# Performance work log

Hardware: AMD Instinct MI355X
Metric: run time of the kernel (lower is better)

## Reference

```python
import jax, jax.numpy as jnp
import numpy as np

E = 262144      # number of edges (triples)
D = 256         # embed_dim
DOUT = 256      # embed_out_dim
NQ = 65536      # num_query (output nodes)
NK = 65536      # num_key
ALPHA = 0.2     # leaky relu slope
EPS = 1e-12


def setup_inputs() -> dict:
    key = jax.random.key(0)
    ks = jax.random.split(key, 7)
    return {
        "key_list": jax.random.randint(ks[0], (E,), 0, NK),
        "key_embed": jax.random.normal(ks[1], (E, D), jnp.float32),
        "query_list": jax.random.randint(ks[2], (E,), 0, NQ),
        "query_embed": jax.random.normal(ks[3], (E, D), jnp.float32),
        # learned parameters (xavier-ish scale)
        "a": jax.random.normal(ks[4], (DOUT, 2 * D), jnp.float32) * 0.05,
        "a_2": jax.random.normal(ks[5], (1, DOUT), jnp.float32) * 0.05,
        "trans": jax.random.normal(ks[6], (DOUT, D), jnp.float32) * 0.05,
    }


def reference(key_list, key_embed, query_list, query_embed, a, a_2, trans):
    # edge_associated_set = trans @ key_embed.T, kept as (E, DOUT)
    edge_assoc = key_embed @ trans.T                              # (E, DOUT)
    # edge_m = a @ cat(key, query).T, kept as (E, DOUT)
    edge_h = jnp.concatenate([key_embed, query_embed], axis=1)    # (E, 2D)
    edge_m = edge_h @ a.T                                         # (E, DOUT)
    powers = -jax.nn.leaky_relu(edge_m @ a_2[0], negative_slope=ALPHA)  # (E,)
    edge_e = jnp.exp(powers)                                      # (E,) unnormalized attn
    # sparse COO sum over key dim == segment-sum by query index
    e_rowsum = jax.ops.segment_sum(edge_e, query_list, num_segments=NQ)[:, None]  # (NQ,1)
    e_rowsum = jnp.where(e_rowsum == 0.0, EPS, e_rowsum)
    # dropout p=0.0 (eval) -> identity
    edge_w = edge_e[:, None] * edge_assoc                         # (E, DOUT)
    h_prime = jax.ops.segment_sum(edge_w, query_list, num_segments=NQ)  # (NQ, DOUT)
    h_prime = h_prime / e_rowsum
    return jax.nn.elu(h_prime)  # concat=True branch
```

## Files before the change

### kernel.cpp

```cpp
#include <hip/hip_runtime.h>
#include <hip/hip_bf16.h>
#include <math.h>

namespace {
constexpr int kD = 256;
constexpr int kDOUT = 256;
constexpr int kNQ = 65536;
constexpr int kE = 262144;
constexpr float kAlpha = 0.2f;
constexpr float kEps = 1e-12f;
constexpr int kCap = 16;
constexpr int kOvfMax = 4096;
}

typedef short bf16x8 __attribute__((ext_vector_type(8)));
typedef float f32x4 __attribute__((ext_vector_type(4)));
typedef unsigned short u16x8 __attribute__((ext_vector_type(8)));

__global__ void compute_c_kernel(const float* __restrict__ a,
                                 const float* __restrict__ a2,
                                 float* __restrict__ c) {
  const int j = blockIdx.x * blockDim.x + threadIdx.x;
  float s = 0.f;
#pragma unroll 8
  for (int k = 0; k < kDOUT; ++k) s = fmaf(a[k * (2 * kD) + j], a2[k], s);
  c[j] = s;
}

__global__ void zero_kernel(int4* __restrict__ p, int* __restrict__ ovf_n) {
  p[blockIdx.x * 256 + threadIdx.x] = int4{0, 0, 0, 0};
  if (blockIdx.x == 0 && threadIdx.x == 0) *ovf_n = 0;
}

__global__ void cvt_trans_kernel(const float* __restrict__ t, ushort* __restrict__ tb) {
  const int i = blockIdx.x * 256 + threadIdx.x;
  const float4 v = reinterpret_cast<const float4*>(t)[i];
  union { ushort4 u; __hip_bfloat16 h[4]; } p;
  p.h[0] = __float2bfloat16(v.x);
  p.h[1] = __float2bfloat16(v.y);
  p.h[2] = __float2bfloat16(v.z);
  p.h[3] = __float2bfloat16(v.w);
  reinterpret_cast<ushort4*>(tb)[i] = p.u;
}

__global__ __launch_bounds__(256) void qdot_bin_kernel(
    const float* __restrict__ query_embed,
    const int* __restrict__ qlist,
    const float* __restrict__ c,
    int* __restrict__ count,
    int2* __restrict__ bins,
    int* __restrict__ ovf_n,
    int* __restrict__ ovf_q,
    int* __restrict__ ovf_e,
    float* __restrict__ ovf_qd) {
  const int wid = threadIdx.x >> 6;
  const int lane = threadIdx.x & 63;
  const int g = lane >> 4;
  const int l4 = lane & 15;
  const int edge = blockIdx.x * 16 + wid * 4 + g;

  int q = 0;
  if (l4 == 0) q = qlist[edge];

  const float4* qr = reinterpret_cast<const float4*>(query_embed) + (size_t)edge * 64 + l4 * 4;
  const float4 r0 = qr[0], r1 = qr[1], r2 = qr[2], r3 = qr[3];
  const float4 c0 = reinterpret_cast<const float4*>(c)[64 + l4 * 4 + 0];
  const float4 c1 = reinterpret_cast<const float4*>(c)[64 + l4 * 4 + 1];
  const float4 c2 = reinterpret_cast<const float4*>(c)[64 + l4 * 4 + 2];
  const float4 c3 = reinterpret_cast<const float4*>(c)[64 + l4 * 4 + 3];

  float s = r0.x * c0.x + r0.y * c0.y + r0.z * c0.z + r0.w * c0.w
          + r1.x * c1.x + r1.y * c1.y + r1.z * c1.z + r1.w * c1.w
          + r2.x * c2.x + r2.y * c2.y + r2.z * c2.z + r2.w * c2.w
          + r3.x * c3.x + r3.y * c3.y + r3.z * c3.z + r3.w * c3.w;
#pragma unroll
  for (int off = 1; off < 16; off <<= 1) s += __shfl_xor(s, off, 64);

  if (l4 == 0) {
    const int slot = atomicAdd(&count[q], 1);
    if (slot < kCap) {
      bins[q * kCap + slot] = make_int2(edge, __float_as_int(s));
    } else {
      const int o = atomicAdd(ovf_n, 1);
      if (o < kOvfMax) { ovf_q[o] = q; ovf_e[o] = edge; ovf_qd[o] = s; }
    }
  }
}

__global__ __launch_bounds__(256) void gather_gemm_kernel(
    const float* __restrict__ key_embed,
    const float* __restrict__ c,
    const int2* __restrict__ bins,
    const int* __restrict__ count,
    const int* __restrict__ ovf_n,
    const int* __restrict__ ovf_q,
    const int* __restrict__ ovf_e,
    const float* __restrict__ ovf_qd,
    const ushort* __restrict__ B,
    float* __restrict__ out) {
  __shared__ ushort A_lds[16][264];
  const int wid = threadIdx.x >> 6;
  const int lane = threadIdx.x & 63;
  const int g = lane >> 4;
  const int l4 = lane & 15;
  const int qloc = wid * 4 + g;
  const int q = blockIdx.x * 16 + qloc;

  const int cnt = count[q];
  const int cm = min(cnt, kCap);
  const int2 mybin = (l4 < cm) ? bins[q * kCap + l4] : make_int2(0, 0);

  const float4 ck0 = reinterpret_cast<const float4*>(c)[l4 * 4 + 0];
  const float4 ck1 = reinterpret_cast<const float4*>(c)[l4 * 4 + 1];
  const float4 ck2 = reinterpret_cast<const float4*>(c)[l4 * 4 + 2];
  const float4 ck3 = reinterpret_cast<const float4*>(c)[l4 * 4 + 3];

  float acc[16] = {};
  float rs = 0.f;

  for (int s = 0; s < cm; s += 4) {
    const int kc = min(4, cm - s);
    float4 r[4][4];
    float qd[4];
#pragma unroll
    for (int t = 0; t < 4; ++t) {
      if (t < kc) {
        const int eg = __shfl(mybin.x, (g << 4) + s + t, 64);
        qd[t] = __int_as_float(__shfl(mybin.y, (g << 4) + s + t, 64));
        const float4* row = reinterpret_cast<const float4*>(key_embed) + (size_t)eg * 64 + l4 * 4;
#pragma unroll
        for (int u = 0; u < 4; ++u) r[t][u] = row[u];
      }
    }
#pragma unroll
    for (int t = 0; t < 4; ++t) {
      if (t < kc) {
        float kd = r[t][0].x * ck0.x + r[t][0].y * ck0.y + r[t][0].z * ck0.z + r[t][0].w * ck0.w
                 + r[t][1].x * ck1.x + r[t][1].y * ck1.y + r[t][1].z * ck1.z + r[t][1].w * ck1.w
                 + r[t][2].x * ck2.x + r[t][2].y * ck2.y + r[t][2].z * ck2.z + r[t][2].w * ck2.w
                 + r[t][3].x * ck3.x + r[t][3].y * ck3.y + r[t][3].z * ck3.z + r[t][3].w * ck3.w;
#pragma unroll
        for (int off = 1; off < 16; off <<= 1) kd += __shfl_xor(kd, off, 64);
        const float sv = kd + qd[t];
        const float p = (sv > 0.f) ? sv : kAlpha * sv;
        const float ev = __expf(-p);
#pragma unroll
        for (int u = 0; u < 4; ++u) {
          acc[u * 4 + 0] = fmaf(ev, r[t][u].x, acc[u * 4 + 0]);
          acc[u * 4 + 1] = fmaf(ev, r[t][u].y, acc[u * 4 + 1]);
          acc[u * 4 + 2] = fmaf(ev, r[t][u].z, acc[u * 4 + 2]);
          acc[u * 4 + 3] = fmaf(ev, r[t][u].w, acc[u * 4 + 3]);
        }
        rs += ev;
      }
    }
  }

  if (cnt > kCap) {
    const int n = min(*ovf_n, kOvfMax);
    for (int i = 0; i < n; ++i) {
      if (ovf_q[i] == q) {
        const float4* row = reinterpret_cast<const float4*>(key_embed) +
                            (size_t)ovf_e[i] * 64 + l4 * 4;
        float4 r4[4];
#pragma unroll
        for (int u = 0; u < 4; ++u) r4[u] = row[u];
        float kd = r4[0].x * ck0.x + r4[0].y * ck0.y + r4[0].z * ck0.z + r4[0].w * ck0.w
                 + r4[1].x * ck1.x + r4[1].y * ck1.y + r4[1].z * ck1.z + r4[1].w * ck1.w
                 + r4[2].x * ck2.x + r4[2].y * ck2.y + r4[2].z * ck2.z + r4[2].w * ck2.w
                 + r4[3].x * ck3.x + r4[3].y * ck3.y + r4[3].z * ck3.z + r4[3].w * ck3.w;
#pragma unroll
        for (int off = 1; off < 16; off <<= 1) kd += __shfl_xor(kd, off, 64);
        const float sv = kd + ovf_qd[i];
        const float p = (sv > 0.f) ? sv : kAlpha * sv;
        const float ev = __expf(-p);
#pragma unroll
        for (int u = 0; u < 4; ++u) {
          acc[u * 4 + 0] = fmaf(ev, r4[u].x, acc[u * 4 + 0]);
          acc[u * 4 + 1] = fmaf(ev, r4[u].y, acc[u * 4 + 1]);
          acc[u * 4 + 2] = fmaf(ev, r4[u].z, acc[u * 4 + 2]);
          acc[u * 4 + 3] = fmaf(ev, r4[u].w, acc[u * 4 + 3]);
        }
        rs += ev;
      }
    }
  }

  const float inv = 1.0f / ((rs == 0.f) ? kEps : rs);
  union { u16x8 u; __hip_bfloat16 h[8]; } p0, p1;
#pragma unroll
  for (int j = 0; j < 8; ++j) p0.h[j] = __float2bfloat16(acc[j] * inv);
#pragma unroll
  for (int j = 0; j < 8; ++j) p1.h[j] = __float2bfloat16(acc[8 + j] * inv);
  *reinterpret_cast<u16x8*>(&A_lds[qloc][l4 * 16]) = p0.u;
  *reinterpret_cast<u16x8*>(&A_lds[qloc][l4 * 16 + 8]) = p1.u;

  __syncthreads();

  const int m = lane & 15;
  const int kb = (lane >> 4) * 8;
  f32x4 acc2[4] = {};

#pragma unroll
  for (int kt = 0; kt < kD; kt += 32) {
    const bf16x8 af = *reinterpret_cast<const bf16x8*>(&A_lds[m][kt + kb]);
#pragma unroll
    for (int nt = 0; nt < 4; ++nt) {
      const int ntg = wid * 4 + nt;
      const bf16x8 bf =
          *reinterpret_cast<const bf16x8*>(&B[(size_t)(ntg * 16 + m) * kD + kt + kb]);
      acc2[nt] = __builtin_amdgcn_mfma_f32_16x16x32_bf16(af, bf, acc2[nt], 0, 0, 0);
    }
  }

#pragma unroll
  for (int nt = 0; nt < 4; ++nt) {
    const int ntg = wid * 4 + nt;
#pragma unroll
    for (int r = 0; r < 4; ++r) {
      const int row = blockIdx.x * 16 + (lane >> 4) * 4 + r;
      const float x = acc2[nt][r];
      out[(size_t)row * kDOUT + ntg * 16 + m] = (x > 0.f) ? x : expm1f(x);
    }
  }
}

extern "C" void kernel_launch(void* const* d_in, const int* in_sizes, int n_in,
                              void* d_out, int out_size, void* d_ws, size_t ws_size,
                              hipStream_t stream) {
  const float* key_embed = (const float*)d_in[1];
  const int* query_list = (const int*)d_in[2];
  const float* query_embed = (const float*)d_in[3];
  const float* a = (const float*)d_in[4];
  const float* a2 = (const float*)d_in[5];
  const float* trans = (const float*)d_in[6];
  float* out = (float*)d_out;

  float* ws = (float*)d_ws;
  float* c = ws;
  int* count = (int*)(c + 512);
  int2* bins = (int2*)(count + kNQ);
  ushort* transb = (ushort*)(bins + (size_t)kNQ * kCap);
  int* ovf_n = (int*)(transb + (size_t)kDOUT * kD);
  int* ovf_q = ovf_n + 4;
  int* ovf_e = ovf_q + kOvfMax;
  float* ovf_qd = (float*)(ovf_e + kOvfMax);

  zero_kernel<<<kNQ / 4 / 256, 256, 0, stream>>>((int4*)count, ovf_n);
  compute_c_kernel<<<2, 256, 0, stream>>>(a, a2, c);
  cvt_trans_kernel<<<kDOUT * kD / 4 / 256, 256, 0, stream>>>(trans, transb);
  qdot_bin_kernel<<<kE / 16, 256, 0, stream>>>(query_embed, query_list, c, count,
                                               bins, ovf_n, ovf_q, ovf_e, ovf_qd);
  gather_gemm_kernel<<<kNQ / 16, 256, 0, stream>>>(key_embed, c, bins, count, ovf_n,
                                                   ovf_q, ovf_e, ovf_qd, transb, out);
}
```

Measured before the change: 213.7 us.

## Merge prep kernels and process 32 queries per gather-GEMM block

```diff
diff --git a/kernel.cpp b/kernel.cpp
--- a/kernel.cpp
+++ b/kernel.cpp
@@ -17,30 +17,35 @@
 typedef float f32x4 __attribute__((ext_vector_type(4)));
 typedef unsigned short u16x8 __attribute__((ext_vector_type(8)));
 
-__global__ void compute_c_kernel(const float* __restrict__ a,
-                                 const float* __restrict__ a2,
-                                 float* __restrict__ c) {
-  const int j = blockIdx.x * blockDim.x + threadIdx.x;
-  float s = 0.f;
+__global__ __launch_bounds__(256) void prep_kernel(
+    const float* __restrict__ a,
+    const float* __restrict__ a2,
+    const float* __restrict__ trans,
+    int4* __restrict__ count4,
+    int* __restrict__ ovf_n,
+    float* __restrict__ c,
+    ushort* __restrict__ tb) {
+  const int b = blockIdx.x;
+  const int tid = threadIdx.x;
+  if (b < 64) {
+    count4[b * 256 + tid] = int4{0, 0, 0, 0};
+    if (b == 0 && tid == 0) *ovf_n = 0;
+  } else if (b < 66) {
+    const int j = (b - 64) * 256 + tid;
+    float s = 0.f;
 #pragma unroll 8
-  for (int k = 0; k < kDOUT; ++k) s = fmaf(a[k * (2 * kD) + j], a2[k], s);
-  c[j] = s;
-}
-
-__global__ void zero_kernel(int4* __restrict__ p, int* __restrict__ ovf_n) {
-  p[blockIdx.x * 256 + threadIdx.x] = int4{0, 0, 0, 0};
-  if (blockIdx.x == 0 && threadIdx.x == 0) *ovf_n = 0;
-}
-
-__global__ void cvt_trans_kernel(const float* __restrict__ t, ushort* __restrict__ tb) {
-  const int i = blockIdx.x * 256 + threadIdx.x;
-  const float4 v = reinterpret_cast<const float4*>(t)[i];
-  union { ushort4 u; __hip_bfloat16 h[4]; } p;
-  p.h[0] = __float2bfloat16(v.x);
-  p.h[1] = __float2bfloat16(v.y);
-  p.h[2] = __float2bfloat16(v.z);
-  p.h[3] = __float2bfloat16(v.w);
-  reinterpret_cast<ushort4*>(tb)[i] = p.u;
+    for (int k = 0; k < kDOUT; ++k) s = fmaf(a[k * (2 * kD) + j], a2[k], s);
+    c[j] = s;
+  } else {
+    const int i = (b - 66) * 256 + tid;
+    const float4 v = reinterpret_cast<const float4*>(trans)[i];
+    union { ushort4 u; __hip_bfloat16 h[4]; } p;
+    p.h[0] = __float2bfloat16(v.x);
+    p.h[1] = __float2bfloat16(v.y);
+    p.h[2] = __float2bfloat16(v.z);
+    p.h[3] = __float2bfloat16(v.w);
+    reinterpret_cast<ushort4*>(tb)[i] = p.u;
+  }
 }
 
 __global__ __launch_bounds__(256) void qdot_bin_kernel(
@@ -98,118 +103,124 @@
     const float* __restrict__ ovf_qd,
     const ushort* __restrict__ B,
     float* __restrict__ out) {
-  __shared__ ushort A_lds[16][264];
+  __shared__ ushort A_lds[32][264];
   const int wid = threadIdx.x >> 6;
   const int lane = threadIdx.x & 63;
   const int g = lane >> 4;
   const int l4 = lane & 15;
-  const int qloc = wid * 4 + g;
-  const int q = blockIdx.x * 16 + qloc;
-
-  const int cnt = count[q];
-  const int cm = min(cnt, kCap);
-  const int2 mybin = (l4 < cm) ? bins[q * kCap + l4] : make_int2(0, 0);
+  const int group = wid * 4 + g;
 
   const float4 ck0 = reinterpret_cast<const float4*>(c)[l4 * 4 + 0];
   const float4 ck1 = reinterpret_cast<const float4*>(c)[l4 * 4 + 1];
   const float4 ck2 = reinterpret_cast<const float4*>(c)[l4 * 4 + 2];
   const float4 ck3 = reinterpret_cast<const float4*>(c)[l4 * 4 + 3];
 
-  float acc[16] = {};
-  float rs = 0.f;
-
-  for (int s = 0; s < cm; s += 4) {
-    const int kc = min(4, cm - s);
-    float4 r[4][4];
-    float qd[4];
-#pragma unroll
-    for (int t = 0; t < 4; ++t) {
-      if (t < kc) {
-        const int eg = __shfl(mybin.x, (g << 4) + s + t, 64);
-        qd[t] = __int_as_float(__shfl(mybin.y, (g << 4) + s + t, 64));
-        const float4* row = reinterpret_cast<const float4*>(key_embed) + (size_t)eg * 64 + l4 * 4;
-#pragma unroll
-        for (int u = 0; u < 4; ++u) r[t][u] = row[u];
+  for (int half = 0; half < 2; ++half) {
+    const int qloc = half * 16 + group;
+    const int q = blockIdx.x * 32 + qloc;
+    const int cnt = count[q];
+    const int cm = min(cnt, kCap);
+    const int2 mybin = (l4 < cm) ? bins[q * kCap + l4] : make_int2(0, 0);
+
+    float acc[16] = {};
+    float rs = 0.f;
+
+    for (int s = 0; s < cm; s += 4) {
+      const int kc = min(4, cm - s);
+      float4 r[4][4];
+      float qd[4];
+#pragma unroll
+      for (int t = 0; t < 4; ++t) {
+        if (t < kc) {
+          const int eg = __shfl(mybin.x, (g << 4) + s + t, 64);
+          qd[t] = __int_as_float(__shfl(mybin.y, (g << 4) + s + t, 64));
+          const float4* row = reinterpret_cast<const float4*>(key_embed) + (size_t)eg * 64 + l4 * 4;
+#pragma unroll
+          for (int u = 0; u < 4; ++u) r[t][u] = row[u];
+        }
       }
-    }
-#pragma unroll
-    for (int t = 0; t < 4; ++t) {
-      if (t < kc) {
-        float kd = r[t][0].x * ck0.x + r[t][0].y * ck0.y + r[t][0].z * ck0.z + r[t][0].w * ck0.w
-                 + r[t][1].x * ck1.x + r[t][1].y * ck1.y + r[t][1].z * ck1.z + r[t][1].w * ck1.w
-                 + r[t][2].x * ck2.x + r[t][2].y * ck2.y + r[t][2].z * ck2.z + r[t][2].w * ck2.w
-                 + r[t][3].x * ck3.x + r[t][3].y * ck3.y + r[t][3].z * ck3.z + r[t][3].w * ck3.w;
-#pragma unroll
-        for (int off = 1; off < 16; off <<= 1) kd += __shfl_xor(kd, off, 64);
-        const float sv = kd + qd[t];
-        const float p = (sv > 0.f) ? sv : kAlpha * sv;
-        const float ev = __expf(-p);
-#pragma unroll
-        for (int u = 0; u < 4; ++u) {
-          acc[u * 4 + 0] = fmaf(ev, r[t][u].x, acc[u * 4 + 0]);
-          acc[u * 4 + 1] = fmaf(ev, r[t][u].y, acc[u * 4 + 1]);
-          acc[u * 4 + 2] = fmaf(ev, r[t][u].z, acc[u * 4 + 2]);
-          acc[u * 4 + 3] = fmaf(ev, r[t][u].w, acc[u * 4 + 3]);
+#pragma unroll
+      for (int t = 0; t < 4; ++t) {
+        if (t < kc) {
+          float kd = r[t][0].x * ck0.x + r[t][0].y * ck0.y + r[t][0].z * ck0.z + r[t][0].w * ck0.w
+                   + r[t][1].x * ck1.x + r[t][1].y * ck1.y + r[t][1].z * ck1.z + r[t][1].w * ck1.w
+                   + r[t][2].x * ck2.x + r[t][2].y * ck2.y + r[t][2].z * ck2.z + r[t][2].w * ck2.w
+                   + r[t][3].x * ck3.x + r[t][3].y * ck3.y + r[t][3].z * ck3.z + r[t][3].w * ck3.w;
+#pragma unroll
+          for (int off = 1; off < 16; off <<= 1) kd += __shfl_xor(kd, off, 64);
+          const float sv = kd + qd[t];
+          const float p = (sv > 0.f) ? sv : kAlpha * sv;
+          const float ev = __expf(-p);
+#pragma unroll
+          for (int u = 0; u < 4; ++u) {
+            acc[u * 4 + 0] = fmaf(ev, r[t][u].x, acc[u * 4 + 0]);
+            acc[u * 4 + 1] = fmaf(ev, r[t][u].y, acc[u * 4 + 1]);
+            acc[u * 4 + 2] = fmaf(ev, r[t][u].z, acc[u * 4 + 2]);
+            acc[u * 4 + 3] = fmaf(ev, r[t][u].w, acc[u * 4 + 3]);
+          }
+          rs += ev;
         }
-        rs += ev;
       }
     }
-  }
-
-  if (cnt > kCap) {
-    const int n = min(*ovf_n, kOvfMax);
-    for (int i = 0; i < n; ++i) {
-      if (ovf_q[i] == q) {
-        const float4* row = reinterpret_cast<const float4*>(key_embed) +
-                            (size_t)ovf_e[i] * 64 + l4 * 4;
-        float4 r4[4];
-#pragma unroll
-        for (int u = 0; u < 4; ++u) r4[u] = row[u];
-        float kd = r4[0].x * ck0.x + r4[0].y * ck0.y + r4[0].z * ck0.z + r4[0].w * ck0.w
-                 + r4[1].x * ck1.x + r4[1].y * ck1.y + r4[1].z * ck1.z + r4[1].w * ck1.w
-                 + r4[2].x * ck2.x + r4[2].y * ck2.y + r4[2].z * ck2.z + r4[2].w * ck2.w
-                 + r4[3].x * ck3.x + r4[3].y * ck3.y + r4[3].z * ck3.z + r4[3].w * ck3.w;
-#pragma unroll
-        for (int off = 1; off < 16; off <<= 1) kd += __shfl_xor(kd, off, 64);
-        const float sv = kd + ovf_qd[i];
-        const float p = (sv > 0.f) ? sv : kAlpha * sv;
-        const float ev = __expf(-p);
-#pragma unroll
-        for (int u = 0; u < 4; ++u) {
-          acc[u * 4 + 0] = fmaf(ev, r4[u].x, acc[u * 4 + 0]);
-          acc[u * 4 + 1] = fmaf(ev, r4[u].y, acc[u * 4 + 1]);
-          acc[u * 4 + 2] = fmaf(ev, r4[u].z, acc[u * 4 + 2]);
-          acc[u * 4 + 3] = fmaf(ev, r4[u].w, acc[u * 4 + 3]);
+
+    if (cnt > kCap) {
+      const int n = min(*ovf_n, kOvfMax);
+      for (int i = 0; i < n; ++i) {
+        if (ovf_q[i] == q) {
+          const float4* row = reinterpret_cast<const float4*>(key_embed) +
+                              (size_t)ovf_e[i] * 64 + l4 * 4;
+          float4 r4[4];
+#pragma unroll
+          for (int u = 0; u < 4; ++u) r4[u] = row[u];
+          float kd = r4[0].x * ck0.x + r4[0].y * ck0.y + r4[0].z * ck0.z + r4[0].w * ck0.w
+                   + r4[1].x * ck1.x + r4[1].y * ck1.y + r4[1].z * ck1.z + r4[1].w * ck1.w
+                   + r4[2].x * ck2.x + r4[2].y * ck2.y + r4[2].z * ck2.z + r4[2].w * ck2.w
+                   + r4[3].x * ck3.x + r4[3].y * ck3.y + r4[3].z * ck3.z + r4[3].w * ck3.w;
+#pragma unroll
+          for (int off = 1; off < 16; off <<= 1) kd += __shfl_xor(kd, off, 64);
+          const float sv = kd + ovf_qd[i];
+          const float p = (sv > 0.f) ? sv : kAlpha * sv;
+          const float ev = __expf(-p);
+#pragma unroll
+          for (int u = 0; u < 4; ++u) {
+            acc[u * 4 + 0] = fmaf(ev, r4[u].x, acc[u * 4 + 0]);
+            acc[u * 4 + 1] = fmaf(ev, r4[u].y, acc[u * 4 + 1]);
+            acc[u * 4 + 2] = fmaf(ev, r4[u].z, acc[u * 4 + 2]);
+            acc[u * 4 + 3] = fmaf(ev, r4[u].w, acc[u * 4 + 3]);
+          }
+          rs += ev;
         }
-        rs += ev;
       }
     }
-  }
-
-  const float inv = 1.0f / ((rs == 0.f) ? kEps : rs);
-  union { u16x8 u; __hip_bfloat16 h[8]; } p0, p1;
-#pragma unroll
-  for (int j = 0; j < 8; ++j) p0.h[j] = __float2bfloat16(acc[j] * inv);
-#pragma unroll
-  for (int j = 0; j < 8; ++j) p1.h[j] = __float2bfloat16(acc[8 + j] * inv);
-  *reinterpret_cast<u16x8*>(&A_lds[qloc][l4 * 16]) = p0.u;
-  *reinterpret_cast<u16x8*>(&A_lds[qloc][l4 * 16 + 8]) = p1.u;
+
+    const float inv = 1.0f / ((rs == 0.f) ? kEps : rs);
+    union { u16x8 u; __hip_bfloat16 h[8]; } p0, p1;
+#pragma unroll
+    for (int j = 0; j < 8; ++j) p0.h[j] = __float2bfloat16(acc[j] * inv);
+#pragma unroll
+    for (int j = 0; j < 8; ++j) p1.h[j] = __float2bfloat16(acc[8 + j] * inv);
+    *reinterpret_cast<u16x8*>(&A_lds[qloc][l4 * 16]) = p0.u;
+    *reinterpret_cast<u16x8*>(&A_lds[qloc][l4 * 16 + 8]) = p1.u;
+  }
 
   __syncthreads();
 
   const int m = lane & 15;
   const int kb = (lane >> 4) * 8;
-  f32x4 acc2[4] = {};
+  f32x4 accA[4] = {};
+  f32x4 accB[4] = {};
 
 #pragma unroll
   for (int kt = 0; kt < kD; kt += 32) {
-    const bf16x8 af = *reinterpret_cast<const bf16x8*>(&A_lds[m][kt + kb]);
+    const bf16x8 af0 = *reinterpret_cast<const bf16x8*>(&A_lds[m][kt + kb]);
+    const bf16x8 af1 = *reinterpret_cast<const bf16x8*>(&A_lds[16 + m][kt + kb]);
 #pragma unroll
     for (int nt = 0; nt < 4; ++nt) {
       const int ntg = wid * 4 + nt;
       const bf16x8 bf =
           *reinterpret_cast<const bf16x8*>(&B[(size_t)(ntg * 16 + m) * kD + kt + kb]);
-      acc2[nt] = __builtin_amdgcn_mfma_f32_16x16x32_bf16(af, bf, acc2[nt], 0, 0, 0);
+      accA[nt] = __builtin_amdgcn_mfma_f32_16x16x32_bf16(af0, bf, accA[nt], 0, 0, 0);
+      accB[nt] = __builtin_amdgcn_mfma_f32_16x16x32_bf16(af1, bf, accB[nt], 0, 0, 0);
     }
   }
 
@@ -218,9 +229,11 @@
     const int ntg = wid * 4 + nt;
 #pragma unroll
     for (int r = 0; r < 4; ++r) {
-      const int row = blockIdx.x * 16 + (lane >> 4) * 4 + r;
-      const float x = acc2[nt][r];
-      out[(size_t)row * kDOUT + ntg * 16 + m] = (x > 0.f) ? x : expm1f(x);
+      const int rbase = blockIdx.x * 32 + (lane >> 4) * 4 + r;
+      const float xa = accA[nt][r];
+      out[(size_t)rbase * kDOUT + ntg * 16 + m] = (xa > 0.f) ? xa : expm1f(xa);
+      const float xb = accB[nt][r];
+      out[(size_t)(rbase + 16) * kDOUT + ntg * 16 + m] = (xb > 0.f) ? xb : expm1f(xb);
     }
   }
 }
@@ -246,11 +259,9 @@
   int* ovf_e = ovf_q + kOvfMax;
   float* ovf_qd = (float*)(ovf_e + kOvfMax);
 
-  zero_kernel<<<kNQ / 4 / 256, 256, 0, stream>>>((int4*)count, ovf_n);
-  compute_c_kernel<<<2, 256, 0, stream>>>(a, a2, c);
-  cvt_trans_kernel<<<kDOUT * kD / 4 / 256, 256, 0, stream>>>(trans, transb);
+  prep_kernel<<<130, 256, 0, stream>>>(a, a2, trans, (int4*)count, ovf_n, c, transb);
   qdot_bin_kernel<<<kE / 16, 256, 0, stream>>>(query_embed, query_list, c, count,
                                                bins, ovf_n, ovf_q, ovf_e, ovf_qd);
-  gather_gemm_kernel<<<kNQ / 16, 256, 0, stream>>>(key_embed, c, bins, count, ovf_n,
+  gather_gemm_kernel<<<kNQ / 32, 256, 0, stream>>>(key_embed, c, bins, count, ovf_n,
                                                    ovf_q, ovf_e, ovf_qd, transb, out);
 }
```

After: 199.6 us. -6.6%, faster.
